# Kernel tuning notes

Measured on AMD Instinct MI355X. Metric: run time of the kernel, lower is better.

Reference implementation:

```python
import jax, jax.numpy as jnp
import numpy as np

EPSILON = 0.1
GAMMA = 1.0
RHO = 0.5
STOPERR = 1e-6
NUMITERMAX = 100
FI = GAMMA / (GAMMA + EPSILON)  # exponent for semi-relaxed KL side


def setup_inputs() -> dict:
    key = jax.random.key(0)
    logits = jax.random.normal(key, (16, 4096, 1024), dtype=jnp.float32)
    return {"logits": logits}


def reference(logits):
    B, n, k = logits.shape
    K = k + 1  # extra 'dustbin' column with zero cost
    cost = -jax.nn.log_softmax(logits, axis=-1)                       # [B,n,k]
    expand_cost = jnp.concatenate([cost, jnp.zeros((B, n, 1), cost.dtype)], axis=-1)
    Q = jnp.exp(-expand_cost / EPSILON)                               # [B,n,K]
    Qt = Q.transpose(0, 2, 1)                                         # [B,K,n]
    Pa = jnp.full((B, n, 1), 1.0 / n, Q.dtype)
    Pb = jnp.full((B, K, 1), RHO / k, Q.dtype).at[:, -1, :].set(1.0 - RHO)
    a0 = jnp.zeros((B, n, 1), Q.dtype)
    b0 = jnp.full((B, K, 1), 1.0 / K, Q.dtype)

    def cond(state):
        _, _, err, it = state
        return jnp.logical_and(err > STOPERR, it < NUMITERMAX)

    def body(state):
        _, b, _, it = state
        a = Pa / jnp.matmul(Q, b)                                     # [B,n,1]
        b_new = Pb / jnp.matmul(Qt, a)                                # [B,K,1]
        b_new = b_new.at[:, :-1, :].set(jnp.power(b_new[:, :-1, :], FI))
        err = jnp.sqrt(jnp.sum((b_new - b) ** 2))
        return (a, b_new, err, it + 1)

    a, b, err, it = jax.lax.while_loop(
        cond, body, (a0, b0, jnp.asarray(1.0, Q.dtype), jnp.asarray(0)))

    plan = a * Q * b.transpose(0, 2, 1) * n                           # [B,n,K]
    return plan[:, :, :-1].astype(jnp.float32)                        # drop dustbin col
```

## Files before the change

kernel.cpp:

```cpp
#include <hip/hip_runtime.h>
#include <hip/hip_bf16.h>
#include <math.h>


namespace {
constexpr int   Bn      = 16;
constexpr int   Kc      = 1024;
constexpr int   KK      = 1025;
constexpr int   BSTR    = 1028;
constexpr int   ROWS    = Bn * 4096;
constexpr int   NBLK    = ROWS / 64;
constexpr float INV_EPS = 10.0f;
constexpr float PA      = 1.0f / 4096.0f;
constexpr float PB_LOW  = (float)(0.5 / 1024.0);
constexpr float PB_DUST = 0.5f;
constexpr float FI_F    = (float)(1.0 / 1.1);
constexpr float STOP    = 1e-6f;
constexpr int   NITER   = 100;
}

typedef __attribute__((ext_vector_type(8))) unsigned short ushort8;

__device__ __forceinline__ float wredsum(float v) {
#pragma unroll
  for (int m = 32; m >= 1; m >>= 1) v += __shfl_xor(v, m, 64);
  return v;
}
__device__ __forceinline__ float wredmax(float v) {
#pragma unroll
  for (int m = 32; m >= 1; m >>= 1) v = fmaxf(v, __shfl_xor(v, m, 64));
  return v;
}
__device__ __forceinline__ unsigned short f2bf(float x) {
  unsigned int u = __float_as_uint(x);
  return (unsigned short)((u + 0x7FFFu + ((u >> 16) & 1u)) >> 16);
}
__device__ __forceinline__ float bf2f(unsigned short h) {
  return __uint_as_float(((unsigned int)h) << 16);
}

__global__ void k_init(float* __restrict__ bvec, int* __restrict__ cnt,
                       int* __restrict__ flag) {
  int tid = blockIdx.x * blockDim.x + threadIdx.x;
  int stride = gridDim.x * blockDim.x;
  for (int i = tid; i < Bn * BSTR; i += stride) {
    int j = i % BSTR;
    bvec[i] = (j < KK) ? (float)(1.0 / 1025.0) : 0.0f;
  }
  if (tid == 0) { *cnt = 0; *flag = 1; }
}

__global__ __launch_bounds__(256) void k_prep(const float* __restrict__ x,
                                              unsigned short* __restrict__ Qb) {
  const int wid = threadIdx.x >> 6, lane = threadIdx.x & 63;
  const int row = blockIdx.x * 4 + wid;
  const float4* xp = (const float4*)(x + ((size_t)row << 10));
  float4 v[4];
#pragma unroll
  for (int s = 0; s < 4; ++s) v[s] = xp[lane * 4 + s];

  float m = -1e30f;
#pragma unroll
  for (int s = 0; s < 4; ++s)
    m = fmaxf(m, fmaxf(fmaxf(v[s].x, v[s].y), fmaxf(v[s].z, v[s].w)));
  m = wredmax(m);

  float sum = 0.0f;
#pragma unroll
  for (int s = 0; s < 4; ++s)
    sum += expf(v[s].x - m) + expf(v[s].y - m) + expf(v[s].z - m) + expf(v[s].w - m);
  sum = wredsum(sum);
  const float lse = m + logf(sum);

  ushort8 q0, q1;
#pragma unroll
  for (int s = 0; s < 2; ++s) {
    q0[s * 4 + 0] = f2bf(expf((v[s].x - lse) * INV_EPS));
    q0[s * 4 + 1] = f2bf(expf((v[s].y - lse) * INV_EPS));
    q0[s * 4 + 2] = f2bf(expf((v[s].z - lse) * INV_EPS));
    q0[s * 4 + 3] = f2bf(expf((v[s].w - lse) * INV_EPS));
  }
#pragma unroll
  for (int s = 0; s < 2; ++s) {
    q1[s * 4 + 0] = f2bf(expf((v[2 + s].x - lse) * INV_EPS));
    q1[s * 4 + 1] = f2bf(expf((v[2 + s].y - lse) * INV_EPS));
    q1[s * 4 + 2] = f2bf(expf((v[2 + s].z - lse) * INV_EPS));
    q1[s * 4 + 3] = f2bf(expf((v[2 + s].w - lse) * INV_EPS));
  }
  ushort8* qp = (ushort8*)(Qb + ((size_t)row << 10));
  qp[lane * 2] = q0;
  qp[lane * 2 + 1] = q1;
}

__global__ __launch_bounds__(256) void k_iter(const unsigned short* __restrict__ Qb,
                                              const float* __restrict__ bvec,
                                              float* __restrict__ avec,
                                              float* __restrict__ part,
                                              float* __restrict__ sumaPart,
                                              const int* __restrict__ flag) {
  if (*flag == 0) return;
  __shared__ float cpart[4][1024];
  __shared__ float sred[4];
  const int wid = threadIdx.x >> 6, lane = threadIdx.x & 63;
  const int baseRow = blockIdx.x * 64;
  const int batch = baseRow >> 12;

  const float4* bp = (const float4*)(bvec + batch * BSTR);
  float4 bb[4];
#pragma unroll
  for (int s = 0; s < 4; ++s) bb[s] = bp[lane * 4 + s];
  const float bdust = bvec[batch * BSTR + 1024];

  float acc[16];
#pragma unroll
  for (int e = 0; e < 16; ++e) acc[e] = 0.0f;
  float sal = 0.0f;

  const int rowBase = baseRow + wid * 16;
#pragma unroll 4
  for (int r = 0; r < 16; ++r) {
    const ushort8* qp = (const ushort8*)(Qb + ((size_t)(rowBase + r) << 10));
    const ushort8 qa = qp[lane * 2], qb = qp[lane * 2 + 1];
    float q[16];
#pragma unroll
    for (int e = 0; e < 8; ++e) { q[e] = bf2f(qa[e]); q[8 + e] = bf2f(qb[e]); }

    float p = 0.0f;
#pragma unroll
    for (int s = 0; s < 4; ++s)
      p += q[s * 4 + 0] * bb[s].x + q[s * 4 + 1] * bb[s].y +
           q[s * 4 + 2] * bb[s].z + q[s * 4 + 3] * bb[s].w;

    const float inner = wredsum(p) + bdust;
    const float a = PA / inner;
    if (lane == 0) { avec[rowBase + r] = a; sal += a; }
#pragma unroll
    for (int e = 0; e < 16; ++e) acc[e] += q[e] * a;
  }
  if (lane == 0) sred[wid] = sal;

  float4* cp = (float4*)&cpart[wid][lane * 16];
#pragma unroll
  for (int s = 0; s < 4; ++s)
    cp[s] = make_float4(acc[s * 4 + 0], acc[s * 4 + 1], acc[s * 4 + 2], acc[s * 4 + 3]);
  __syncthreads();

  const int j = threadIdx.x * 4;
  const float4 s0 = *(const float4*)&cpart[0][j];
  const float4 s1 = *(const float4*)&cpart[1][j];
  const float4 s2 = *(const float4*)&cpart[2][j];
  const float4 s3 = *(const float4*)&cpart[3][j];
  float4 o;
  o.x = s0.x + s1.x + s2.x + s3.x;
  o.y = s0.y + s1.y + s2.y + s3.y;
  o.z = s0.z + s1.z + s2.z + s3.z;
  o.w = s0.w + s1.w + s2.w + s3.w;
  ((float4*)(part + ((size_t)blockIdx.x << 10)))[threadIdx.x] = o;
  if (threadIdx.x == 0)
    sumaPart[blockIdx.x] = sred[0] + sred[1] + sred[2] + sred[3];
}

__global__ __launch_bounds__(1024) void k_fin(float* __restrict__ bvec,
                                              const float* __restrict__ part,
                                              const float* __restrict__ sumaPart,
                                              float* __restrict__ e2Part,
                                              int* __restrict__ cnt,
                                              int* __restrict__ flag) {
  if (*flag == 0) return;
  const int b = blockIdx.x;
  const int t = threadIdx.x;

  const float* pp = part + ((size_t)b << 16);
  float s = 0.0f;
#pragma unroll 8
  for (int blk = 0; blk < 64; ++blk) s += pp[blk * 1024 + t];

  const float bold = bvec[b * BSTR + t];
  const float bnew = exp2f(FI_F * log2f(PB_LOW / s));
  bvec[b * BSTR + t] = bnew;
  float e2 = (bnew - bold) * (bnew - bold);

  if (t < 64) {
    float sa = wredsum(sumaPart[b * 64 + t]);
    if (t == 0) {
      const float bo = bvec[b * BSTR + 1024];
      const float bn = PB_DUST / sa;
      bvec[b * BSTR + 1024] = bn;
      e2 += (bn - bo) * (bn - bo);
    }
  }

  __shared__ float red[16];
  const float v = wredsum(e2);
  if ((t & 63) == 0) red[t >> 6] = v;
  __syncthreads();
  if (t == 0) {
    float tt = 0.0f;
    for (int w = 0; w < 16; ++w) tt += red[w];
    e2Part[b] = tt;
    __threadfence();
    const int old = atomicAdd(cnt, 1);
    if (old == Bn - 1) {
      __threadfence();
      float tot = 0.0f;
      for (int w = 0; w < Bn; ++w) tot += e2Part[w];
      const float err = sqrtf(tot);
      if (!(err > STOP)) *flag = 0;
      *cnt = 0;
    }
  }
}

__global__ __launch_bounds__(256) void k_plan(const float* __restrict__ x,
                                              float* __restrict__ out,
                                              const float* __restrict__ avec,
                                              const float* __restrict__ bvec) {
  const int wid = threadIdx.x >> 6, lane = threadIdx.x & 63;
  const int row = blockIdx.x * 4 + wid;
  const int batch = row >> 12;
  const float4* xp = (const float4*)(x + ((size_t)row << 10));
  float4 v[4];
#pragma unroll
  for (int s = 0; s < 4; ++s) v[s] = xp[lane * 4 + s];

  float m = -1e30f;
#pragma unroll
  for (int s = 0; s < 4; ++s)
    m = fmaxf(m, fmaxf(fmaxf(v[s].x, v[s].y), fmaxf(v[s].z, v[s].w)));
  m = wredmax(m);
  float sum = 0.0f;
#pragma unroll
  for (int s = 0; s < 4; ++s)
    sum += expf(v[s].x - m) + expf(v[s].y - m) + expf(v[s].z - m) + expf(v[s].w - m);
  sum = wredsum(sum);
  const float lse = m + logf(sum);

  const float sc = avec[row] * 4096.0f;
  const float4* bp = (const float4*)(bvec + batch * BSTR);
  float4* op = (float4*)(out + ((size_t)row << 10));
#pragma unroll
  for (int s = 0; s < 4; ++s) {
    const float4 b = bp[lane * 4 + s];
    float4 o;
    o.x = expf((v[s].x - lse) * INV_EPS) * sc * b.x;
    o.y = expf((v[s].y - lse) * INV_EPS) * sc * b.y;
    o.z = expf((v[s].z - lse) * INV_EPS) * sc * b.z;
    o.w = expf((v[s].w - lse) * INV_EPS) * sc * b.w;
    op[lane * 4 + s] = o;
  }
}

extern "C" void kernel_launch(void* const* d_in, const int* in_sizes, int n_in,
                              void* d_out, int out_size, void* d_ws, size_t ws_size,
                              hipStream_t stream) {
  const float* logits = (const float*)d_in[0];
  unsigned short* Qb = (unsigned short*)d_out;
  float* ws = (float*)d_ws;
  float* bvec     = ws;
  float* avec     = bvec + Bn * BSTR;
  float* part     = avec + ROWS;
  float* sumaPart = part + (size_t)NBLK * Kc;
  float* e2Part   = sumaPart + NBLK;
  int*   cnt      = (int*)(e2Part + Bn);
  int*   flag     = cnt + 1;

  k_init<<<64, 256, 0, stream>>>(bvec, cnt, flag);
  k_prep<<<ROWS / 4, 256, 0, stream>>>(logits, Qb);
  for (int it = 0; it < NITER; ++it) {
    k_iter<<<NBLK, 256, 0, stream>>>(Qb, bvec, avec, part, sumaPart, flag);
    k_fin<<<Bn, 1024, 0, stream>>>(bvec, part, sumaPart, e2Part, cnt, flag);
  }
  k_plan<<<ROWS / 4, 256, 0, stream>>>(logits, (float*)d_out, avec, bvec);
}
```

Measured before the change: 3.243 ms.

## Fuse b-update into iteration kernel via last-blocks ticket reduction, fuse prep into first iteration

Removes the separate k_fin launch per iteration. The last 256 blocks to finish, identified by an atomic ticket counter, spin-wait until all partials are written. They then reduce columns, update b and accumulate the error atomically. The Q precompute (softmax + exp + bf16 pack) is also folded into the first iteration kernel, so logits are read once without a separate launch. This halves the launch count and removes the low-parallelism 16-block finisher. The cost is spin-waiting, which relies on all blocks being co-resident or scheduled, and relaxed atomics for visibility.

```diff
diff --git a/kernel.cpp b/kernel.cpp
--- a/kernel.cpp
+++ b/kernel.cpp
@@ -1,5 +1,4 @@
 #include <hip/hip_runtime.h>
-#include <hip/hip_bf16.h>
 #include <math.h>
 
 
@@ -8,8 +7,9 @@
 constexpr int   Kc      = 1024;
 constexpr int   KK      = 1025;
 constexpr int   BSTR    = 1028;
-constexpr int   ROWS    = Bn * 4096;
-constexpr int   NBLK    = ROWS / 64;
+constexpr int   ROWS    = 65536;
+constexpr int   NBLK    = 1024;
+constexpr int   NFIN    = 256;
 constexpr float INV_EPS = 10.0f;
 constexpr float PA      = 1.0f / 4096.0f;
 constexpr float PB_LOW  = (float)(0.5 / 1024.0);
@@ -21,6 +21,9 @@
 
 typedef __attribute__((ext_vector_type(8))) unsigned short ushort8;
 
+#define LOADX(p)    __hip_atomic_load((p), __ATOMIC_RELAXED, __HIP_MEMORY_SCOPE_AGENT)
+#define STOREX(p,v) __hip_atomic_store((p), (v), __ATOMIC_RELAXED, __HIP_MEMORY_SCOPE_AGENT)
+
 __device__ __forceinline__ float wredsum(float v) {
 #pragma unroll
   for (int m = 32; m >= 1; m >>= 1) v += __shfl_xor(v, m, 64);
@@ -39,7 +42,8 @@
   return __uint_as_float(((unsigned int)h) << 16);
 }
 
-__global__ void k_init(float* __restrict__ bvec, int* __restrict__ cnt,
+__global__ void k_init(float* __restrict__ bvec, float* __restrict__ e2acc,
+                       int* __restrict__ cnt, int* __restrict__ cnt2,
                        int* __restrict__ flag) {
   int tid = blockIdx.x * blockDim.x + threadIdx.x;
   int stride = gridDim.x * blockDim.x;
@@ -47,62 +51,29 @@
     int j = i % BSTR;
     bvec[i] = (j < KK) ? (float)(1.0 / 1025.0) : 0.0f;
   }
-  if (tid == 0) { *cnt = 0; *flag = 1; }
-}
-
-__global__ __launch_bounds__(256) void k_prep(const float* __restrict__ x,
-                                              unsigned short* __restrict__ Qb) {
-  const int wid = threadIdx.x >> 6, lane = threadIdx.x & 63;
-  const int row = blockIdx.x * 4 + wid;
-  const float4* xp = (const float4*)(x + ((size_t)row << 10));
-  float4 v[4];
-#pragma unroll
-  for (int s = 0; s < 4; ++s) v[s] = xp[lane * 4 + s];
-
-  float m = -1e30f;
-#pragma unroll
-  for (int s = 0; s < 4; ++s)
-    m = fmaxf(m, fmaxf(fmaxf(v[s].x, v[s].y), fmaxf(v[s].z, v[s].w)));
-  m = wredmax(m);
-
-  float sum = 0.0f;
-#pragma unroll
-  for (int s = 0; s < 4; ++s)
-    sum += expf(v[s].x - m) + expf(v[s].y - m) + expf(v[s].z - m) + expf(v[s].w - m);
-  sum = wredsum(sum);
-  const float lse = m + logf(sum);
-
-  ushort8 q0, q1;
-#pragma unroll
-  for (int s = 0; s < 2; ++s) {
-    q0[s * 4 + 0] = f2bf(expf((v[s].x - lse) * INV_EPS));
-    q0[s * 4 + 1] = f2bf(expf((v[s].y - lse) * INV_EPS));
-    q0[s * 4 + 2] = f2bf(expf((v[s].z - lse) * INV_EPS));
-    q0[s * 4 + 3] = f2bf(expf((v[s].w - lse) * INV_EPS));
-  }
-#pragma unroll
-  for (int s = 0; s < 2; ++s) {
-    q1[s * 4 + 0] = f2bf(expf((v[2 + s].x - lse) * INV_EPS));
-    q1[s * 4 + 1] = f2bf(expf((v[2 + s].y - lse) * INV_EPS));
-    q1[s * 4 + 2] = f2bf(expf((v[2 + s].z - lse) * INV_EPS));
-    q1[s * 4 + 3] = f2bf(expf((v[2 + s].w - lse) * INV_EPS));
-  }
-  ushort8* qp = (ushort8*)(Qb + ((size_t)row << 10));
-  qp[lane * 2] = q0;
-  qp[lane * 2 + 1] = q1;
-}
-
-__global__ __launch_bounds__(256) void k_iter(const unsigned short* __restrict__ Qb,
-                                              const float* __restrict__ bvec,
-                                              float* __restrict__ avec,
-                                              float* __restrict__ part,
-                                              float* __restrict__ sumaPart,
-                                              const int* __restrict__ flag) {
-  if (*flag == 0) return;
+  for (int i = tid; i < NITER; i += stride) {
+    e2acc[i] = 0.0f; cnt[i] = 0; cnt2[i] = 0;
+  }
+  if (tid == 0) *flag = 1;
+}
+
+template <bool FIRST>
+__global__ __launch_bounds__(256, 4) void k_iter(
+    const float* __restrict__ x, unsigned short* __restrict__ Qb,
+    float* __restrict__ bvec, float* __restrict__ avec,
+    float* __restrict__ part, float* __restrict__ sumaPart,
+    float* __restrict__ e2acc, int* __restrict__ cnt, int* __restrict__ cnt2,
+    int* __restrict__ flag, int it) {
   __shared__ float cpart[4][1024];
   __shared__ float sred[4];
-  const int wid = threadIdx.x >> 6, lane = threadIdx.x & 63;
-  const int baseRow = blockIdx.x * 64;
+  __shared__ int shi;
+  const int tid = threadIdx.x, wid = tid >> 6, lane = tid & 63;
+  if (tid == 0) shi = *flag;
+  __syncthreads();
+  if (shi == 0) return;
+
+  const int blk = blockIdx.x;
+  const int baseRow = blk * 64;
   const int batch = baseRow >> 12;
 
   const float4* bp = (const float4*)(bvec + batch * BSTR);
@@ -119,11 +90,42 @@
   const int rowBase = baseRow + wid * 16;
 #pragma unroll 4
   for (int r = 0; r < 16; ++r) {
-    const ushort8* qp = (const ushort8*)(Qb + ((size_t)(rowBase + r) << 10));
-    const ushort8 qa = qp[lane * 2], qb = qp[lane * 2 + 1];
     float q[16];
-#pragma unroll
-    for (int e = 0; e < 8; ++e) { q[e] = bf2f(qa[e]); q[8 + e] = bf2f(qb[e]); }
+    if constexpr (FIRST) {
+      const float4* xp = (const float4*)(x + ((size_t)(rowBase + r) << 10));
+      float4 v[4];
+#pragma unroll
+      for (int s = 0; s < 4; ++s) v[s] = xp[lane * 4 + s];
+      float m = -1e30f;
+#pragma unroll
+      for (int s = 0; s < 4; ++s)
+        m = fmaxf(m, fmaxf(fmaxf(v[s].x, v[s].y), fmaxf(v[s].z, v[s].w)));
+      m = wredmax(m);
+      float su = 0.0f;
+#pragma unroll
+      for (int s = 0; s < 4; ++s)
+        su += expf(v[s].x - m) + expf(v[s].y - m) + expf(v[s].z - m) + expf(v[s].w - m);
+      su = wredsum(su);
+      const float lse = m + logf(su);
+      ushort8 qa, qb2;
+#pragma unroll
+      for (int s = 0; s < 4; ++s) {
+        const unsigned short u0 = f2bf(expf((v[s].x - lse) * INV_EPS));
+        const unsigned short u1 = f2bf(expf((v[s].y - lse) * INV_EPS));
+        const unsigned short u2 = f2bf(expf((v[s].z - lse) * INV_EPS));
+        const unsigned short u3 = f2bf(expf((v[s].w - lse) * INV_EPS));
+        if (s < 2) { qa[s*4+0]=u0; qa[s*4+1]=u1; qa[s*4+2]=u2; qa[s*4+3]=u3; }
+        else { qb2[(s-2)*4+0]=u0; qb2[(s-2)*4+1]=u1; qb2[(s-2)*4+2]=u2; qb2[(s-2)*4+3]=u3; }
+        q[s*4+0]=bf2f(u0); q[s*4+1]=bf2f(u1); q[s*4+2]=bf2f(u2); q[s*4+3]=bf2f(u3);
+      }
+      ushort8* qp = (ushort8*)(Qb + ((size_t)(rowBase + r) << 10));
+      qp[lane * 2] = qa; qp[lane * 2 + 1] = qb2;
+    } else {
+      const ushort8* qp = (const ushort8*)(Qb + ((size_t)(rowBase + r) << 10));
+      const ushort8 qa = qp[lane * 2], qb2 = qp[lane * 2 + 1];
+#pragma unroll
+      for (int e = 0; e < 8; ++e) { q[e] = bf2f(qa[e]); q[8 + e] = bf2f(qb2[e]); }
+    }
 
     float p = 0.0f;
 #pragma unroll
@@ -145,68 +147,68 @@
     cp[s] = make_float4(acc[s * 4 + 0], acc[s * 4 + 1], acc[s * 4 + 2], acc[s * 4 + 3]);
   __syncthreads();
 
-  const int j = threadIdx.x * 4;
-  const float4 s0 = *(const float4*)&cpart[0][j];
-  const float4 s1 = *(const float4*)&cpart[1][j];
-  const float4 s2 = *(const float4*)&cpart[2][j];
-  const float4 s3 = *(const float4*)&cpart[3][j];
-  float4 o;
-  o.x = s0.x + s1.x + s2.x + s3.x;
-  o.y = s0.y + s1.y + s2.y + s3.y;
-  o.z = s0.z + s1.z + s2.z + s3.z;
-  o.w = s0.w + s1.w + s2.w + s3.w;
-  ((float4*)(part + ((size_t)blockIdx.x << 10)))[threadIdx.x] = o;
-  if (threadIdx.x == 0)
-    sumaPart[blockIdx.x] = sred[0] + sred[1] + sred[2] + sred[3];
-}
-
-__global__ __launch_bounds__(1024) void k_fin(float* __restrict__ bvec,
-                                              const float* __restrict__ part,
-                                              const float* __restrict__ sumaPart,
-                                              float* __restrict__ e2Part,
-                                              int* __restrict__ cnt,
-                                              int* __restrict__ flag) {
-  if (*flag == 0) return;
-  const int b = blockIdx.x;
-  const int t = threadIdx.x;
-
-  const float* pp = part + ((size_t)b << 16);
-  float s = 0.0f;
-#pragma unroll 8
-  for (int blk = 0; blk < 64; ++blk) s += pp[blk * 1024 + t];
-
-  const float bold = bvec[b * BSTR + t];
-  const float bnew = exp2f(FI_F * log2f(PB_LOW / s));
-  bvec[b * BSTR + t] = bnew;
-  float e2 = (bnew - bold) * (bnew - bold);
-
-  if (t < 64) {
-    float sa = wredsum(sumaPart[b * 64 + t]);
-    if (t == 0) {
-      const float bo = bvec[b * BSTR + 1024];
-      const float bn = PB_DUST / sa;
-      bvec[b * BSTR + 1024] = bn;
-      e2 += (bn - bo) * (bn - bo);
-    }
-  }
-
-  __shared__ float red[16];
-  const float v = wredsum(e2);
-  if ((t & 63) == 0) red[t >> 6] = v;
-  __syncthreads();
-  if (t == 0) {
-    float tt = 0.0f;
-    for (int w = 0; w < 16; ++w) tt += red[w];
-    e2Part[b] = tt;
-    __threadfence();
-    const int old = atomicAdd(cnt, 1);
-    if (old == Bn - 1) {
-      __threadfence();
-      float tot = 0.0f;
-      for (int w = 0; w < Bn; ++w) tot += e2Part[w];
-      const float err = sqrtf(tot);
-      if (!(err > STOP)) *flag = 0;
-      *cnt = 0;
+  {
+    const int j = tid * 4;
+    float* pb = part + ((size_t)blk << 10) + j;
+#pragma unroll
+    for (int e = 0; e < 4; ++e) {
+      const float v = cpart[0][j + e] + cpart[1][j + e] + cpart[2][j + e] + cpart[3][j + e];
+      STOREX(pb + e, v);
+    }
+    if (tid == 0)
+      STOREX(&sumaPart[blk], sred[0] + sred[1] + sred[2] + sred[3]);
+  }
+  __syncthreads();
+  if (tid == 0)
+    shi = __hip_atomic_fetch_add(&cnt[it], 1, __ATOMIC_RELAXED, __HIP_MEMORY_SCOPE_AGENT);
+  __syncthreads();
+  const int ticket = shi;
+  if (ticket < NBLK - NFIN) return;
+
+  if (tid == 0) {
+    while (LOADX(&cnt[it]) < NBLK) __builtin_amdgcn_s_sleep(1);
+  }
+  __syncthreads();
+
+  const int fin_id = ticket - (NBLK - NFIN);
+  const int fb = fin_id >> 4;
+  const int colBase = (fin_id & 15) * 64;
+  {
+    const float* basep = part + (((size_t)(fb * 64 + wid * 16)) << 10) + colBase + lane;
+    float s = 0.0f;
+#pragma unroll
+    for (int j = 0; j < 16; ++j) s += LOADX(basep + ((size_t)j << 10));
+    cpart[wid][lane] = s;
+  }
+  __syncthreads();
+  if (wid == 0) {
+    const int col = colBase + lane;
+    const float s = cpart[0][lane] + cpart[1][lane] + cpart[2][lane] + cpart[3][lane];
+    float* bslot = bvec + fb * BSTR + col;
+    const float bold = *bslot;
+    const float bnew = exp2f(FI_F * log2f(PB_LOW / s));
+    *bslot = bnew;
+    float e2 = (bnew - bold) * (bnew - bold);
+
+    if ((fin_id & 15) == 0) {
+      float sa = LOADX(&sumaPart[fb * 64 + lane]);
+      sa = wredsum(sa);
+      if (lane == 0) {
+        float* ds = bvec + fb * BSTR + 1024;
+        const float bo = *ds;
+        const float bn = PB_DUST / sa;
+        *ds = bn;
+        e2 += (bn - bo) * (bn - bo);
+      }
+    }
+    const float e2w = wredsum(e2);
+    if (lane == 0) {
+      __hip_atomic_fetch_add(&e2acc[it], e2w, __ATOMIC_RELAXED, __HIP_MEMORY_SCOPE_AGENT);
+      const int t2 = __hip_atomic_fetch_add(&cnt2[it], 1, __ATOMIC_ACQ_REL, __HIP_MEMORY_SCOPE_AGENT);
+      if (t2 == NFIN - 1) {
+        const float err = sqrtf(LOADX(&e2acc[it]));
+        if (!(err > STOP)) STOREX(flag, 0);
+      }
     }
   }
 }
@@ -260,15 +262,16 @@
   float* avec     = bvec + Bn * BSTR;
   float* part     = avec + ROWS;
   float* sumaPart = part + (size_t)NBLK * Kc;
-  float* e2Part   = sumaPart + NBLK;
-  int*   cnt      = (int*)(e2Part + Bn);
-  int*   flag     = cnt + 1;
-
-  k_init<<<64, 256, 0, stream>>>(bvec, cnt, flag);
-  k_prep<<<ROWS / 4, 256, 0, stream>>>(logits, Qb);
-  for (int it = 0; it < NITER; ++it) {
-    k_iter<<<NBLK, 256, 0, stream>>>(Qb, bvec, avec, part, sumaPart, flag);
-    k_fin<<<Bn, 1024, 0, stream>>>(bvec, part, sumaPart, e2Part, cnt, flag);
-  }
+  float* e2acc    = sumaPart + NBLK;
+  int*   cnt      = (int*)(e2acc + NITER);
+  int*   cnt2     = cnt + NITER;
+  int*   flag     = cnt2 + NITER;
+
+  k_init<<<64, 256, 0, stream>>>(bvec, e2acc, cnt, cnt2, flag);
+  k_iter<true><<<NBLK, 256, 0, stream>>>(logits, Qb, bvec, avec, part, sumaPart,
+                                         e2acc, cnt, cnt2, flag, 0);
+  for (int it = 1; it < NITER; ++it)
+    k_iter<false><<<NBLK, 256, 0, stream>>>(logits, Qb, bvec, avec, part, sumaPart,
+                                            e2acc, cnt, cnt2, flag, it);
   k_plan<<<ROWS / 4, 256, 0, stream>>>(logits, (float*)d_out, avec, bvec);
 }
```

After: 5.344 ms. 1.65x slower.
